# Optimization experiments

Measured on AMD Instinct MI355X. Metric: run time of the kernel, lower is better.

The kernel has to match this reference:

```python
import jax, jax.numpy as jnp
import numpy as np

# SLAYER neuron / simulation constants (from netParams yaml)
THETA = 10.0      # spike threshold
TAU_SR = 10.0     # PSP (SRM) time constant, ms
TS = 1.0          # simulation time step, ms
TAU_RHO = 1.0     # surrogate-gradient width
SCALE_RHO = 1.0   # surrogate-gradient scale
N_TIME_BINS = 300 # tSample / Ts


@jax.custom_vjp
def spike_fn(u):
    # Hard threshold forward; surrogate gradient backward (SLAYER escape-rate pdf).
    return (u >= THETA).astype(u.dtype)

def _spike_fwd(u):
    return spike_fn(u), u

def _spike_bwd(u, g):
    return (g * SCALE_RHO * jnp.exp(-jnp.abs(u - THETA) / TAU_RHO),)

spike_fn.defvjp(_spike_fwd, _spike_bwd)


def psp(x):
    # Causal leaky-integrator (first-order SRM) filter over time.
    # x: [B, T, F] -> u[t] = decay * u[t-1] + x[t]
    decay = jnp.exp(jnp.asarray(-TS / TAU_SR, x.dtype))
    xT = jnp.swapaxes(x, 0, 1)  # [T, B, F]
    def step(u, xt):
        u = decay * u + xt
        return u, u
    _, out = jax.lax.scan(step, jnp.zeros_like(xT[0]), xT)
    return jnp.swapaxes(out, 0, 1)  # [B, T, F]


def rate_encode(inp, n_time_bins, key):
    # Bernoulli rate coding: spike prob per time bin = pixel intensity in [0,1].
    # inp: [B, C, H, W] -> spikes: [B, T, C*H*W]
    B = inp.shape[0]
    probs = inp.reshape(B, 1, -1)  # [B, 1, F]
    u = jax.random.uniform(key, (B, n_time_bins, probs.shape[-1]), dtype=inp.dtype)
    return (u < probs).astype(inp.dtype)


def setup_inputs() -> dict:
    key = jax.random.key(0)
    k1, k2, k3 = jax.random.split(key, 3)
    B, C, H, W = 32, 3, 32, 32
    F_in, F_hid, F_out = C * H * W, 410, 10
    inp = jax.random.uniform(k1, (B, C, H, W), dtype=jnp.float32)
    W1 = jax.random.normal(k2, (F_hid, F_in), dtype=jnp.float32) / np.sqrt(F_in).astype(np.float32)
    W2 = jax.random.normal(k3, (F_out, F_hid), dtype=jnp.float32) / np.sqrt(F_hid).astype(np.float32)
    return {"inp": inp, "W1": W1, "W2": W2}


def reference(inp, W1, W2):
    spikes = rate_encode(inp, N_TIME_BINS, jax.random.key(42))   # [B, T, 3072]
    a1 = jnp.einsum('btf,of->bto', spikes, W1)                    # dense per time bin
    s1 = spike_fn(psp(a1))                                        # [B, T, 410]
    a2 = jnp.einsum('btf,of->bto', s1, W2)
    s2 = spike_fn(psp(a2))                                        # [B, T, 10]
    return jnp.swapaxes(s2, 1, 2)                                 # [B, 10, T]
```

## Files before the change

kernel.cpp:

```cpp
#include <hip/hip_runtime.h>
#include <stdint.h>

#define B_SZ 32
#define T_SZ 300
#define F_IN 3072
#define F_HID 410
#define F_OUT 10
#define M_SZ (B_SZ * T_SZ)
#define N_PAD 448
#define KW (F_IN / 32)
#define TOTAL_ELEMS (B_SZ * T_SZ * F_IN)
#define N_WORDS (TOTAL_ELEMS / 32)
#define A2_STRIDE 16
#define NCHUNK 10
#define CLEN 30
#define NKB (F_IN / 256)
#define MT_CNT (M_SZ / 64)
#define W1_BLOCKS 672
#define RNG_BLOCKS 14400

#define DECAY 0.90483741803595957f
#define THETA 10.0f
#define KS2 (0x1BD11BDAu ^ 42u)

typedef __attribute__((ext_vector_type(8))) int i32x8;
typedef __attribute__((ext_vector_type(16))) float f32x16;

#define TF_R(r) { x0 += x1; \
  asm("v_alignbit_b32 %0, %0, %0, %1" : "+v"(x1) : "n"(32 - (r))); \
  x1 ^= x0; }

__device__ __forceinline__ uint32_t tf_bits(uint32_t x1i) {
  uint32_t x0 = 0u, x1 = x1i;
  TF_R(13) TF_R(15) TF_R(26) TF_R(6)
  x0 += 42u; x1 += KS2 + 1u;
  TF_R(17) TF_R(29) TF_R(16) TF_R(24)
  x0 += KS2; x1 += 2u;
  TF_R(13) TF_R(15) TF_R(26) TF_R(6)
  x1 += 42u + 3u;
  TF_R(17) TF_R(29) TF_R(16) TF_R(24)
  x0 += 42u; x1 += KS2 + 4u;
  TF_R(13) TF_R(15) TF_R(26) TF_R(6)
  x0 += KS2; x1 += 5u;
  return x0 ^ x1;
}

__device__ __forceinline__ void gld16(const void* g, void* l) {
  __builtin_amdgcn_global_load_lds(
      (const __attribute__((address_space(1))) uint32_t*)g,
      (__attribute__((address_space(3))) uint32_t*)l, 16, 0, 0);
}

__global__ __launch_bounds__(256) void prep(const float* __restrict__ inp,
                                            const float* __restrict__ W1,
                                            uint8_t* __restrict__ W1s,
                                            uint32_t* __restrict__ sbitsT) {
  if (blockIdx.x < W1_BLOCKS) {
    int idx = blockIdx.x * 256 + threadIdx.x;
    int g = idx * 8;
    int n = g / F_IN;
    int k = g - n * F_IN;
    uint32_t d0 = 0u, d1 = 0u;
    if (n < F_HID) {
      const float* s = W1 + (size_t)n * F_IN + k;
      float4 v0 = ((const float4*)s)[0];
      float4 v1 = ((const float4*)s)[1];
      int t0 = __builtin_amdgcn_cvt_pk_fp8_f32(v0.x, v0.y, 0, false);
      t0 = __builtin_amdgcn_cvt_pk_fp8_f32(v0.z, v0.w, t0, true);
      int t1 = __builtin_amdgcn_cvt_pk_fp8_f32(v1.x, v1.y, 0, false);
      t1 = __builtin_amdgcn_cvt_pk_fp8_f32(v1.z, v1.w, t1, true);
      d0 = (uint32_t)t0; d1 = (uint32_t)t1;
    }
    int nt = n >> 6, r = n & 63;
    int kb = k >> 8, c = (k >> 4) & 15, half = (k >> 3) & 1;
    size_t dst = ((((size_t)nt * NKB + kb) * 64 + r) * 16 + (c ^ (r & 15))) * 16 + half * 8;
    *(uint2*)(W1s + dst) = make_uint2(d0, d1);
  } else {
    uint32_t idx = (blockIdx.x - W1_BLOCKS) * 256u + threadIdx.x;
    uint32_t q = idx & 3u;
    uint32_t j = idx >> 2;
    uint32_t r = j & 63u;
    uint32_t t1 = j >> 6;
    uint32_t wi = t1 & 7u;
    uint32_t t2 = t1 >> 3;
    uint32_t kb = t2 % (uint32_t)NKB;
    uint32_t mt = t2 / (uint32_t)NKB;
    uint32_t m = mt * 64u + r;
    uint32_t b = m / (uint32_t)T_SZ;
    uint32_t f = (kb * 8u + wi) * 32u + q * 8u;
    const float* p = inp + b * F_IN + f;
    float4 va = ((const float4*)p)[0];
    float4 vb = ((const float4*)p)[1];
    uint32_t T0 = (uint32_t)ceilf(va.x * 8388608.0f);
    uint32_t T1 = (uint32_t)ceilf(va.y * 8388608.0f);
    uint32_t T2 = (uint32_t)ceilf(va.z * 8388608.0f);
    uint32_t T3 = (uint32_t)ceilf(va.w * 8388608.0f);
    uint32_t T4 = (uint32_t)ceilf(vb.x * 8388608.0f);
    uint32_t T5 = (uint32_t)ceilf(vb.y * 8388608.0f);
    uint32_t T6 = (uint32_t)ceilf(vb.z * 8388608.0f);
    uint32_t T7 = (uint32_t)ceilf(vb.w * 8388608.0f);
    uint32_t b42 = m * (uint32_t)F_IN + f + 42u;
    uint32_t w = 0u;
#define GEN(jj, Tn) { uint32_t bits = tf_bits(b42 + (jj)); \
  w |= ((bits >> 9) < (Tn)) ? (1u << (jj)) : 0u; }
    GEN(0, T0) GEN(1, T1) GEN(2, T2) GEN(3, T3)
    GEN(4, T4) GEN(5, T5) GEN(6, T6) GEN(7, T7)
#undef GEN
    ((uint8_t*)sbitsT)[idx] = (uint8_t)w;
  }
}

__global__ __launch_bounds__(256) void gemm1(const uint32_t* __restrict__ sbitsT,
                                             const uint8_t* __restrict__ W1s,
                                             float* __restrict__ a1) {
  __shared__ uint32_t sAT[8 * 64];
  __shared__ uint8_t sB[64 * 256];

  const int tid = threadIdx.x;
  const int mtile = blockIdx.x;
  const int nt = blockIdx.y;
  const int m0 = mtile * 64;
  const int n0 = nt * 64;
  const int wv = tid >> 6, lane = tid & 63;
  const int wm = (wv & 1) * 32, wn = (wv >> 1) * 32;
  const int l31 = lane & 31, lh = lane >> 5;

  const uint8_t* gB0 = W1s + (size_t)nt * NKB * 16384;
  const uint8_t* gA0 = (const uint8_t*)sbitsT + (size_t)mtile * NKB * 2048;

  f32x16 acc;
#pragma unroll
  for (int e = 0; e < 16; ++e) acc[e] = 0.0f;

  for (int kb = 0; kb < NKB; ++kb) {
    const uint8_t* gB = gB0 + (size_t)kb * 16384;
#pragma unroll
    for (int q = 0; q < 4; ++q)
      gld16(gB + (wv * 4 + q) * 1024 + lane * 16, &sB[(wv * 4 + q) * 1024]);
    if (wv < 2)
      gld16(gA0 + (size_t)kb * 2048 + wv * 1024 + lane * 16,
            (uint8_t*)sAT + wv * 1024);
    __syncthreads();
#pragma unroll
    for (int sub = 0; sub < 4; ++sub) {
      int row = wn + l31;
      int cb = sub * 4 + lh * 2;
      uint4 u0 = *(uint4*)&sB[row * 256 + (((cb + 0) ^ (row & 15)) << 4)];
      uint4 u1 = *(uint4*)&sB[row * 256 + (((cb + 1) ^ (row & 15)) << 4)];
      i32x8 bfr;
      bfr[0] = u0.x; bfr[1] = u0.y; bfr[2] = u0.z; bfr[3] = u0.w;
      bfr[4] = u1.x; bfr[5] = u1.y; bfr[6] = u1.z; bfr[7] = u1.w;
      uint32_t w = sAT[(sub * 2 + lh) * 64 + wm + l31];
      i32x8 afr;
#pragma unroll
      for (int j = 0; j < 8; ++j) {
        uint32_t n = (w >> (4 * j)) & 15u;
        afr[j] = (int)(((n * 0x204081u) & 0x01010101u) * 0x38u);
      }
      acc = __builtin_amdgcn_mfma_scale_f32_32x32x64_f8f6f4(
          afr, bfr, acc, 0, 0, 0, 127, 0, 127);
    }
    __syncthreads();
  }
  int col = n0 + wn + l31;
#pragma unroll
  for (int rg = 0; rg < 16; ++rg) {
    int row = m0 + wm + (rg & 3) + 8 * (rg >> 2) + 4 * lh;
    a1[(size_t)row * N_PAD + col] = acc[rg];
  }
}

__global__ __launch_bounds__(256) void psp1_partial(float* __restrict__ a1,
                                                    float* __restrict__ fin) {
  int idx = blockIdx.x * 256 + threadIdx.x;
  if (idx >= B_SZ * NCHUNK * N_PAD) return;
  int o = idx % N_PAD;
  int bc = idx / N_PAD;
  int c = bc % NCHUNK;
  int b = bc / NCHUNK;
  float* p = a1 + ((size_t)(b * T_SZ + c * CLEN)) * N_PAD + o;
  float u = 0.0f;
#pragma unroll
  for (int i = 0; i < CLEN; ++i) {
    u = __fadd_rn(__fmul_rn(DECAY, u), p[(size_t)i * N_PAD]);
    p[(size_t)i * N_PAD] = u;
  }
  fin[(size_t)bc * N_PAD + o] = u;
}

__global__ __launch_bounds__(256) void apply_gemm2(const float* __restrict__ a1,
                                                   const float* __restrict__ fin,
                                                   const float* __restrict__ W2,
                                                   float* __restrict__ a2) {
  __shared__ float sW2[F_OUT * F_HID];
  for (int i = threadIdx.x; i < F_OUT * F_HID; i += 256) sW2[i] = W2[i];
  __syncthreads();
  int m = blockIdx.x * 4 + (threadIdx.x >> 6);
  int lane = threadIdx.x & 63;
  int b = m / T_SZ, t = m % T_SZ;
  int c = t / CLEN, tl = t % CLEN;
  float d30 = 1.0f;
#pragma unroll
  for (int i = 0; i < CLEN; ++i) d30 *= DECAY;
  float dp = DECAY;
  for (int i = 0; i < tl; ++i) dp *= DECAY;
  float p[F_OUT];
#pragma unroll
  for (int o = 0; o < F_OUT; ++o) p[o] = 0.0f;
#pragma unroll
  for (int j = 0; j < 7; ++j) {
    int hh = lane + j * 64;
    float u = a1[(size_t)m * N_PAD + hh];
    if (c > 0) {
      float F = 0.0f;
      const float* f = fin + (size_t)b * NCHUNK * N_PAD + hh;
      for (int cc = 0; cc < c; ++cc)
        F = f[(size_t)cc * N_PAD] + d30 * F;
      u = __fadd_rn(u, __fmul_rn(dp, F));
    }
    bool valid = hh < F_HID;
    float s = (u >= THETA && valid) ? 1.0f : 0.0f;
    int hcl = valid ? hh : 0;
#pragma unroll
    for (int o = 0; o < F_OUT; ++o) p[o] = fmaf(s, sW2[o * F_HID + hcl], p[o]);
  }
#pragma unroll
  for (int o = 0; o < F_OUT; ++o)
#pragma unroll
    for (int s = 1; s < 64; s <<= 1) p[o] += __shfl_xor(p[o], s, 64);
  if (lane < F_OUT) a2[(size_t)m * A2_STRIDE + lane] = p[lane];
}

__global__ __launch_bounds__(128) void psp2(const float* __restrict__ a2,
                                            float* __restrict__ out) {
  __shared__ float chf[NCHUNK][F_OUT];
  __shared__ float seed[NCHUNK][F_OUT];
  int b = blockIdx.x;
  int tid = threadIdx.x;
  int o = tid / NCHUNK, c = tid % NCHUNK;
  const float* p = a2 + ((size_t)(b * T_SZ + c * CLEN)) * A2_STRIDE + o;
  float v[CLEN];
  float pa[CLEN];
  if (tid < F_OUT * NCHUNK) {
#pragma unroll
    for (int i = 0; i < CLEN; ++i) v[i] = p[(size_t)i * A2_STRIDE];
    float u = 0.0f;
#pragma unroll
    for (int i = 0; i < CLEN; ++i) {
      u = __fadd_rn(__fmul_rn(DECAY, u), v[i]);
      pa[i] = u;
    }
    chf[c][o] = u;
  }
  __syncthreads();
  if (tid < F_OUT) {
    float d30 = 1.0f;
#pragma unroll
    for (int i = 0; i < CLEN; ++i) d30 *= DECAY;
    float F = 0.0f;
    for (int cc = 0; cc < NCHUNK; ++cc) {
      F = chf[cc][tid] + d30 * F;
      seed[cc][tid] = F;
    }
  }
  __syncthreads();
  if (tid < F_OUT * NCHUNK) {
    float F = (c == 0) ? 0.0f : seed[c - 1][o];
    float dp = DECAY;
    float* q = out + (size_t)b * F_OUT * T_SZ + (size_t)o * T_SZ + c * CLEN;
#pragma unroll
    for (int i = 0; i < CLEN; ++i) {
      float u = (c == 0) ? pa[i] : __fadd_rn(pa[i], __fmul_rn(dp, F));
      q[i] = (u >= THETA) ? 1.0f : 0.0f;
      dp *= DECAY;
    }
  }
}

extern "C" void kernel_launch(void* const* d_in, const int* in_sizes, int n_in,
                              void* d_out, int out_size, void* d_ws, size_t ws_size,
                              hipStream_t stream) {
  const float* inp = (const float*)d_in[0];
  const float* W1  = (const float*)d_in[1];
  const float* W2  = (const float*)d_in[2];
  float* out = (float*)d_out;
  char* ws = (char*)d_ws;
  uint8_t* W1s = (uint8_t*)(ws);
  uint32_t* sbitsT = (uint32_t*)(ws + 1376256);
  float* a1 = (float*)(ws + 1376256 + 3686400);
  float* fin = a1 + (size_t)M_SZ * N_PAD;
  float* a2 = fin + (size_t)B_SZ * NCHUNK * N_PAD;

  prep<<<dim3(W1_BLOCKS + RNG_BLOCKS), dim3(256), 0, stream>>>(inp, W1, W1s, sbitsT);
  gemm1<<<dim3(MT_CNT, N_PAD / 64), dim3(256), 0, stream>>>(sbitsT, W1s, a1);
  psp1_partial<<<dim3((B_SZ * NCHUNK * N_PAD) / 256), dim3(256), 0, stream>>>(a1, fin);
  apply_gemm2<<<dim3(M_SZ / 4), dim3(256), 0, stream>>>(a1, fin, W2, a2);
  psp2<<<dim3(B_SZ), dim3(128), 0, stream>>>(a2, out);
}
```

Baseline: 173.8 us.

## Double-buffer gemm1 shared tiles and precompute chunk carry prefix scan

The main GEMM now stages the next k-block of weights and spike bits into a second LDS buffer while the current block feeds the MFMAs, aiming to hide global-load latency behind compute. A new small kernel turns the per-chunk PSP end values into an exclusive prefix over chunks in place. apply_gemm2 then reads one carry value per element instead of re-running a loop over earlier chunks. The trade-off is doubled LDS use, which may reduce occupancy, and one extra kernel launch.

New measurement: 165.6 us. 1.05x faster.

```diff
diff --git a/kernel.cpp b/kernel.cpp
--- a/kernel.cpp
+++ b/kernel.cpp
@@ -113,8 +113,8 @@
 __global__ __launch_bounds__(256) void gemm1(const uint32_t* __restrict__ sbitsT,
                                              const uint8_t* __restrict__ W1s,
                                              float* __restrict__ a1) {
-  __shared__ uint32_t sAT[8 * 64];
-  __shared__ uint8_t sB[64 * 256];
+  __shared__ uint32_t sAT[2][8 * 64];
+  __shared__ uint8_t sB[2][64 * 256];
 
   const int tid = threadIdx.x;
   const int mtile = blockIdx.x;
@@ -128,29 +128,37 @@
   const uint8_t* gB0 = W1s + (size_t)nt * NKB * 16384;
   const uint8_t* gA0 = (const uint8_t*)sbitsT + (size_t)mtile * NKB * 2048;
 
-  f32x16 acc;
-#pragma unroll
-  for (int e = 0; e < 16; ++e) acc[e] = 0.0f;
-
-  for (int kb = 0; kb < NKB; ++kb) {
+  auto STAGE = [&](int buf, int kb) {
     const uint8_t* gB = gB0 + (size_t)kb * 16384;
 #pragma unroll
     for (int q = 0; q < 4; ++q)
-      gld16(gB + (wv * 4 + q) * 1024 + lane * 16, &sB[(wv * 4 + q) * 1024]);
+      gld16(gB + (wv * 4 + q) * 1024 + lane * 16, &sB[buf][(wv * 4 + q) * 1024]);
     if (wv < 2)
       gld16(gA0 + (size_t)kb * 2048 + wv * 1024 + lane * 16,
-            (uint8_t*)sAT + wv * 1024);
-    __syncthreads();
+            (uint8_t*)&sAT[buf][0] + wv * 1024);
+  };
+
+  f32x16 acc;
+#pragma unroll
+  for (int e = 0; e < 16; ++e) acc[e] = 0.0f;
+
+  STAGE(0, 0);
+  __syncthreads();
+  int cur = 0;
+  for (int kb = 0; kb < NKB; ++kb) {
+    if (kb + 1 < NKB) STAGE(cur ^ 1, kb + 1);
+    const uint8_t* sBc = sB[cur];
+    const uint32_t* sATc = sAT[cur];
 #pragma unroll
     for (int sub = 0; sub < 4; ++sub) {
       int row = wn + l31;
       int cb = sub * 4 + lh * 2;
-      uint4 u0 = *(uint4*)&sB[row * 256 + (((cb + 0) ^ (row & 15)) << 4)];
-      uint4 u1 = *(uint4*)&sB[row * 256 + (((cb + 1) ^ (row & 15)) << 4)];
+      uint4 u0 = *(uint4*)&sBc[row * 256 + (((cb + 0) ^ (row & 15)) << 4)];
+      uint4 u1 = *(uint4*)&sBc[row * 256 + (((cb + 1) ^ (row & 15)) << 4)];
       i32x8 bfr;
       bfr[0] = u0.x; bfr[1] = u0.y; bfr[2] = u0.z; bfr[3] = u0.w;
       bfr[4] = u1.x; bfr[5] = u1.y; bfr[6] = u1.z; bfr[7] = u1.w;
-      uint32_t w = sAT[(sub * 2 + lh) * 64 + wm + l31];
+      uint32_t w = sATc[(sub * 2 + lh) * 64 + wm + l31];
       i32x8 afr;
 #pragma unroll
       for (int j = 0; j < 8; ++j) {
@@ -161,6 +169,7 @@
           afr, bfr, acc, 0, 0, 0, 127, 0, 127);
     }
     __syncthreads();
+    cur ^= 1;
   }
   int col = n0 + wn + l31;
 #pragma unroll
@@ -186,6 +195,27 @@
     p[(size_t)i * N_PAD] = u;
   }
   fin[(size_t)bc * N_PAD + o] = u;
+}
+
+__global__ __launch_bounds__(256) void fscan(float* __restrict__ fin) {
+  int idx = blockIdx.x * 256 + threadIdx.x;
+  if (idx >= B_SZ * N_PAD) return;
+  int o = idx % N_PAD;
+  int b = idx / N_PAD;
+  float* f = fin + (size_t)b * NCHUNK * N_PAD + o;
+  float d30 = 1.0f;
+#pragma unroll
+  for (int i = 0; i < CLEN; ++i) d30 *= DECAY;
+  float v[NCHUNK - 1];
+#pragma unroll
+  for (int c = 0; c < NCHUNK - 1; ++c) v[c] = f[(size_t)c * N_PAD];
+  float F = 0.0f;
+  f[0] = 0.0f;
+#pragma unroll
+  for (int c = 1; c < NCHUNK; ++c) {
+    F = v[c - 1] + d30 * F;
+    f[(size_t)c * N_PAD] = F;
+  }
 }
 
 __global__ __launch_bounds__(256) void apply_gemm2(const float* __restrict__ a1,
@@ -199,11 +229,9 @@
   int lane = threadIdx.x & 63;
   int b = m / T_SZ, t = m % T_SZ;
   int c = t / CLEN, tl = t % CLEN;
-  float d30 = 1.0f;
-#pragma unroll
-  for (int i = 0; i < CLEN; ++i) d30 *= DECAY;
   float dp = DECAY;
   for (int i = 0; i < tl; ++i) dp *= DECAY;
+  const float* frow = fin + (size_t)(b * NCHUNK + c) * N_PAD;
   float p[F_OUT];
 #pragma unroll
   for (int o = 0; o < F_OUT; ++o) p[o] = 0.0f;
@@ -212,10 +240,7 @@
     int hh = lane + j * 64;
     float u = a1[(size_t)m * N_PAD + hh];
     if (c > 0) {
-      float F = 0.0f;
-      const float* f = fin + (size_t)b * NCHUNK * N_PAD + hh;
-      for (int cc = 0; cc < c; ++cc)
-        F = f[(size_t)cc * N_PAD] + d30 * F;
+      float F = frow[hh];
       u = __fadd_rn(u, __fmul_rn(dp, F));
     }
     bool valid = hh < F_HID;
@@ -294,6 +319,7 @@
   prep<<<dim3(W1_BLOCKS + RNG_BLOCKS), dim3(256), 0, stream>>>(inp, W1, W1s, sbitsT);
   gemm1<<<dim3(MT_CNT, N_PAD / 64), dim3(256), 0, stream>>>(sbitsT, W1s, a1);
   psp1_partial<<<dim3((B_SZ * NCHUNK * N_PAD) / 256), dim3(256), 0, stream>>>(a1, fin);
+  fscan<<<dim3((B_SZ * N_PAD) / 256), dim3(256), 0, stream>>>(fin);
   apply_gemm2<<<dim3(M_SZ / 4), dim3(256), 0, stream>>>(a1, fin, W2, a2);
   psp2<<<dim3(B_SZ), dim3(128), 0, stream>>>(a2, out);
 }
```
